# Kernel optimization log

Measured on AMD Instinct MI355X. Metric: run time of the kernel, lower is better.

## Reference

```python
import jax, jax.numpy as jnp
import numpy as np
from functools import partial

NUM_HEADS = 12
RATIO_ACT = 0.5   # prune_ratio_act_store
RATIO_ATTN = 0.5  # prune_ratio_attn_mat_store


def kth_mask(x, ratio):
    # torch.kthvalue semantics: threshold = k-th SMALLEST of |x| over the flat tensor
    n = x.size
    k = int(np.clip(n * ratio, 1, n))
    mag = jnp.abs(x)
    thr = jnp.sort(mag.reshape(-1))[k - 1]
    return (mag >= thr).astype(x.dtype)


def st(dense, prune):
    # straight-through: value = dense, gradient flows through `prune` path
    return jax.lax.stop_gradient(dense) + prune - jax.lax.stop_gradient(prune)


def _softmax_prune_impl(x, ratio):
    dense = jax.nn.softmax(x, axis=-1)
    mask = kth_mask(dense, ratio)
    return dense, mask * dense


@partial(jax.custom_vjp, nondiff_argnums=(1,))
def softmax_prune(x, ratio):
    return _softmax_prune_impl(x, ratio)


def _sp_fwd(x, ratio):
    dense, sparse = _softmax_prune_impl(x, ratio)
    return (dense, sparse), sparse


def _sp_bwd(ratio, A, cots):
    # custom backward uses the SPARSE probs in the softmax Jacobian; the
    # cotangent of the sparse output is ignored (matches the torch Function)
    g_dense, _ = cots
    g = A * (g_dense - jnp.sum(g_dense * A, axis=-1, keepdims=True))
    return (g,)


softmax_prune.defvjp(_sp_fwd, _sp_bwd)


def setup_inputs() -> dict:
    key = jax.random.key(0)
    ks = jax.random.split(key, 5)
    B, S, H = 8, 577, 768
    hs = jax.random.normal(ks[0], (B, S, H), dtype=jnp.float32)
    w = lambda k: jax.random.normal(k, (H, H), dtype=jnp.float32) * 0.02
    z = jnp.zeros((H,), dtype=jnp.float32)
    return {
        "hidden_states": hs,
        "Wq": w(ks[1]), "bq": z,
        "Wk": w(ks[2]), "bk": z,
        "Wv": w(ks[3]), "bv": z,
        "Wo": w(ks[4]), "bo": z,
    }


def attention_forward(hidden_states, Wq, bq, Wk, bk, Wv, bv, Wo, bo):
    B, S, H = hidden_states.shape
    nh, hd = NUM_HEADS, H // NUM_HEADS
    sg = jax.lax.stop_gradient
    lin = lambda x, W, b: x @ W + b

    # prune hidden states by global magnitude threshold
    hs_p = sg(kth_mask(hidden_states, RATIO_ACT)) * hidden_states

    q = st(lin(hidden_states, Wq, bq), lin(hs_p, Wq, bq))
    k = st(lin(hidden_states, Wk, bk), lin(hs_p, Wk, bk))
    v = st(lin(hidden_states, Wv, bv), lin(hs_p, Wv, bv))

    heads = lambda x: x.reshape(B, S, nh, hd).transpose(0, 2, 1, 3)  # [B,h,S,d]
    q, k, v = heads(q), heads(k), heads(v)

    qp = sg(kth_mask(q, RATIO_ACT)) * q
    kp = sg(kth_mask(k, RATIO_ACT)) * k

    scores = st(jnp.einsum('bhqd,bhkd->bhqk', q, k),
                jnp.einsum('bhqd,bhkd->bhqk', qp, kp))
    scores = scores / float(np.sqrt(hd))

    probs, probs_p = softmax_prune(scores, RATIO_ATTN)  # dropout rate = 0 -> identity

    vp = sg(kth_mask(v, RATIO_ACT)) * v
    ctx = st(jnp.einsum('bhqk,bhkd->bhqd', probs, v),
             jnp.einsum('bhqk,bhkd->bhqd', probs_p, vp))

    ctx = ctx.transpose(0, 2, 1, 3).reshape(B, S, H)
    ctx_p = sg(kth_mask(ctx, RATIO_ACT)) * ctx

    out = st(lin(ctx, Wo, bo), lin(ctx_p, Wo, bo))
    return out  # vis=False -> weights is None


def reference(hidden_states, Wq, bq, Wk, bk, Wv, bv, Wo, bo):
    return attention_forward(hidden_states, Wq, bq, Wk, bk, Wv, bv, Wo, bo)
```

## Files before the change

kernel.cpp:

```cpp
#include <hip/hip_runtime.h>
#include <hip/hip_bf16.h>


#define B_ 8
#define S_ 577
#define H_ 768
#define NH_ 12
#define HD_ 64
#define M_ (B_*S_)
#define MPAD 4736
#define BH_ (B_*NH_)
#define SKPAD 640
#define LTS 136
#define LTS2 264

typedef __attribute__((ext_vector_type(8))) short short8;
typedef __attribute__((ext_vector_type(4))) short s16x4;
typedef __attribute__((ext_vector_type(4))) float f32x4;

__device__ inline unsigned short f2bf(float f){
    unsigned int u = __float_as_uint(f);
    u = u + 0x7fffu + ((u>>16)&1u);
    return (unsigned short)(u>>16);
}

__device__ inline void gload_lds16(const short* g, short* l){
    __builtin_amdgcn_global_load_lds((const __attribute__((address_space(1))) void*)g,
                                     (__attribute__((address_space(3))) void*)l, 16, 0, 0);
}

__global__ __launch_bounds__(256) void k_prep(
    const float* __restrict__ hs, short* __restrict__ abf,
    const float* __restrict__ Wq, const float* __restrict__ Wk,
    const float* __restrict__ Wv, const float* __restrict__ Wo,
    short* __restrict__ Tq, short* __restrict__ Tk,
    short* __restrict__ Tv, short* __restrict__ To,
    short* __restrict__ kh, short* __restrict__ vt)
{
    const int bid = blockIdx.x, t = threadIdx.x;
    if(bid < 1776){
        int i = bid*256 + t;
        if(bid >= 1731){ *(short8*)(abf + (size_t)i*8) = (short8){}; return; }
        const float4* p = (const float4*)(hs + (size_t)i*8);
        float4 a = p[0], b = p[1];
        short8 v;
        v[0]=(short)f2bf(a.x); v[1]=(short)f2bf(a.y); v[2]=(short)f2bf(a.z); v[3]=(short)f2bf(a.w);
        v[4]=(short)f2bf(b.x); v[5]=(short)f2bf(b.y); v[6]=(short)f2bf(b.z); v[7]=(short)f2bf(b.w);
        *(short8*)(abf + (size_t)i*8) = v;
    } else if(bid < 2352){
        int zidx = bid - 1776;
        int z = zidx & 3, rem = zidx >> 2;
        int kx = rem % 12, ny = rem / 12;
        const float* W = z==0?Wq: z==1?Wk: z==2?Wv:Wo;
        short*       T = z==0?Tq: z==1?Tk: z==2?Tv:To;
        __shared__ float lds[64][65];
        int k0 = kx*64, n0 = ny*64;
        for(int i=0;i<4;i++){
            int row = i*16 + (t>>4);
            int col = (t&15)*4;
            float4 v = *(const float4*)&W[(k0+row)*768 + n0 + col];
            lds[row][col]=v.x; lds[row][col+1]=v.y; lds[row][col+2]=v.z; lds[row][col+3]=v.w;
        }
        __syncthreads();
        for(int i=0;i<4;i++){
            int n = i*16 + (t>>4);
            int k4 = (t&15)*4;
            for(int j=0;j<4;j++)
                T[(n0+n)*768 + k0 + k4 + j] = (short)f2bf(lds[k4+j][n]);
        }
    } else {
        int tid = (bid-2352)*256 + t;
        short8 z = {};
        if(tid < 48384){
            int row_id = tid>>3, ch = tid&7;
            int bh = row_id/63, r = row_id - bh*63;
            *(short8*)&kh[((size_t)bh*SKPAD + 577 + r)*64 + ch*8] = z;
        } else if(tid < 97536){
            int j = tid - 48384;
            int row_id = j>>3, ch = j&7;
            int bh = row_id>>6, d = row_id&63;
            *(short8*)&vt[((size_t)bh*64 + d)*SKPAD + 576 + ch*8] = z;
        }
    }
}

__global__ __launch_bounds__(512) void k_qkv(
    const short* __restrict__ A, const short* __restrict__ T,
    const float* __restrict__ b0, const float* __restrict__ b1, const float* __restrict__ b2,
    short* __restrict__ oq, short* __restrict__ ok, short* __restrict__ ovt)
{
    __shared__ short sh[65536];
    const int t = threadIdx.x;

    const int nwg = gridDim.x;
    const int q8 = nwg>>3, r8 = nwg&7;
    const int xcd = blockIdx.x&7, cidx = blockIdx.x>>3;
    const int wg = (xcd<r8 ? xcd*(q8+1) : r8*(q8+1) + (xcd-r8)*q8) + cidx;
    const int mt = wg/9, nt9 = wg - mt*9;
    const int m0 = mt*256, n0 = nt9*256;
    const int seg = n0/768;
    const float* bias = (seg==0?b0: seg==1?b1:b2);
    const int nlb = n0 - seg*768;

    const int w = t>>6, lane = t&63, g = lane>>4, c = lane&15;
    const int wm = w>>2, wn = w&3;

    const int srow = t>>3, sch = t&7;
    const int sx = (sch ^ (srow&7))*8;
    const short* pa[2][2]; const short* pb[2][2];
    #pragma unroll
    for(int hf=0; hf<2; hf++)
        #pragma unroll
        for(int i=0;i<2;i++){
            int rga = m0 + hf*128 + i*64 + srow;
            if(rga > 4735) rga = 4735;
            pa[hf][i] = A + (size_t)rga*768 + sx;
            pb[hf][i] = T + (size_t)(n0 + hf*128 + i*64 + srow)*768 + sx;
        }
    const int dof = srow*64 + sch*8;

    f32x4 acc[8][4] = {};

    #define STAGE(tt) { int pS = ((tt)&1)*16384; int kof = (tt)*64;              \
        _Pragma("unroll") for(int hf=0; hf<2; hf++){                             \
            _Pragma("unroll") for(int i=0;i<2;i++){                              \
                gload_lds16(pa[hf][i] + kof, &sh[pS + hf*8192 + i*4096 + dof]);  \
                gload_lds16(pb[hf][i] + kof, &sh[32768 + pS + hf*8192 + i*4096 + dof]); } } }

    STAGE(0);
    asm volatile("s_waitcnt vmcnt(0)" ::: "memory");
    __builtin_amdgcn_s_barrier();
    asm volatile("" ::: "memory");

    for(int kt=0; kt<12; kt++){
        const int p = (kt&1)*16384;
        const short* LA = &sh[p + wm*8192];
        const short* LB = &sh[32768 + p + (wn>>1)*8192];
        const int brow0 = (wn&1)*64;

        short8 af[4][2], af2[4][2], bfv[4][2];
        #pragma unroll
        for(int mi=0; mi<4; mi++){
            int rih = mi*16 + c, rx = (rih&7)<<3;
            af[mi][0] = *(const short8*)&LA[rih*64 + ((g*8) ^ rx)];
            af[mi][1] = *(const short8*)&LA[rih*64 + ((32+g*8) ^ rx)];
        }
        #pragma unroll
        for(int ni=0; ni<2; ni++){
            int rih = brow0 + ni*16 + c, rx = (rih&7)<<3;
            bfv[ni][0] = *(const short8*)&LB[rih*64 + ((g*8) ^ rx)];
            bfv[ni][1] = *(const short8*)&LB[rih*64 + ((32+g*8) ^ rx)];
        }
        if(kt < 11) STAGE(kt+1);
        __builtin_amdgcn_s_barrier();
        asm volatile("s_waitcnt lgkmcnt(0)" ::: "memory");
        __builtin_amdgcn_s_setprio(1);
        #pragma unroll
        for(int mi=0; mi<4; mi++)
            #pragma unroll
            for(int ni=0; ni<2; ni++){
                acc[mi][ni] = __builtin_amdgcn_mfma_f32_16x16x32_bf16(af[mi][0], bfv[ni][0], acc[mi][ni], 0,0,0);
                acc[mi][ni] = __builtin_amdgcn_mfma_f32_16x16x32_bf16(af[mi][1], bfv[ni][1], acc[mi][ni], 0,0,0);
            }
        __builtin_amdgcn_s_setprio(0);
        __builtin_amdgcn_s_barrier();
        asm volatile("" ::: "memory");

        #pragma unroll
        for(int ni=2; ni<4; ni++){
            int rih = brow0 + ni*16 + c, rx = (rih&7)<<3;
            bfv[ni][0] = *(const short8*)&LB[rih*64 + ((g*8) ^ rx)];
            bfv[ni][1] = *(const short8*)&LB[rih*64 + ((32+g*8) ^ rx)];
        }
        __builtin_amdgcn_s_barrier();
        asm volatile("s_waitcnt lgkmcnt(0)" ::: "memory");
        __builtin_amdgcn_s_setprio(1);
        #pragma unroll
        for(int mi=0; mi<4; mi++)
            #pragma unroll
            for(int ni=2; ni<4; ni++){
                acc[mi][ni] = __builtin_amdgcn_mfma_f32_16x16x32_bf16(af[mi][0], bfv[ni][0], acc[mi][ni], 0,0,0);
                acc[mi][ni] = __builtin_amdgcn_mfma_f32_16x16x32_bf16(af[mi][1], bfv[ni][1], acc[mi][ni], 0,0,0);
            }
        __builtin_amdgcn_s_setprio(0);
        __builtin_amdgcn_s_barrier();
        asm volatile("" ::: "memory");

        #pragma unroll
        for(int mi=0; mi<4; mi++){
            int rih = 64 + mi*16 + c, rx = (rih&7)<<3;
            af2[mi][0] = *(const short8*)&LA[rih*64 + ((g*8) ^ rx)];
            af2[mi][1] = *(const short8*)&LA[rih*64 + ((32+g*8) ^ rx)];
        }
        __builtin_amdgcn_s_barrier();
        asm volatile("s_waitcnt lgkmcnt(0)" ::: "memory");
        __builtin_amdgcn_s_setprio(1);
        #pragma unroll
        for(int mi=0; mi<4; mi++)
            #pragma unroll
            for(int ni=0; ni<2; ni++){
                acc[4+mi][ni] = __builtin_amdgcn_mfma_f32_16x16x32_bf16(af2[mi][0], bfv[ni][0], acc[4+mi][ni], 0,0,0);
                acc[4+mi][ni] = __builtin_amdgcn_mfma_f32_16x16x32_bf16(af2[mi][1], bfv[ni][1], acc[4+mi][ni], 0,0,0);
            }
        __builtin_amdgcn_s_setprio(0);
        __builtin_amdgcn_s_barrier();
        asm volatile("" ::: "memory");

        __builtin_amdgcn_s_setprio(1);
        #pragma unroll
        for(int mi=0; mi<4; mi++)
            #pragma unroll
            for(int ni=2; ni<4; ni++){
                acc[4+mi][ni] = __builtin_amdgcn_mfma_f32_16x16x32_bf16(af2[mi][0], bfv[ni][0], acc[4+mi][ni], 0,0,0);
                acc[4+mi][ni] = __builtin_amdgcn_mfma_f32_16x16x32_bf16(af2[mi][1], bfv[ni][1], acc[4+mi][ni], 0,0,0);
            }
        __builtin_amdgcn_s_setprio(0);
        asm volatile("s_waitcnt vmcnt(0)" ::: "memory");
        __builtin_amdgcn_s_barrier();
        asm volatile("" ::: "memory");
    }
    #undef STAGE

    if(seg==2){
        #pragma unroll
        for(int cch=0; cch<2; cch++){
            if((wn>>1) == cch){
                #pragma unroll
                for(int mi=0; mi<8; mi++)
                    #pragma unroll
                    for(int ni=0; ni<4; ni++){
                        int nc = (wn&1)*64 + ni*16 + c;
                        float bv = bias[nlb + cch*128 + nc];
                        s16x4 pk;
                        #pragma unroll
                        for(int r=0;r<4;r++) pk[r] = (short)f2bf(acc[mi][ni][r] + bv);
                        int ml0 = wm*128 + mi*16 + g*4;
                        *(s16x4*)&sh[nc*LTS2 + ml0] = pk;
                    }
            }
            __syncthreads();
            #pragma unroll
            for(int i=0;i<8;i++){
                int idx = i*512 + t;
                int rp = idx>>5, ch = idx&31;
                short8 v8 = *(const short8*)&sh[rp*LTS2 + ch*8];
                int nl = nlb + cch*128 + rp, hh = nl>>6, dd = nl&63;
                int mg = m0 + ch*8;
                if(mg < M_){
                    int bb = mg/S_, s0 = mg - bb*S_;
                    if(s0+7 < S_ && mg+7 < M_){
                        *(short8*)&ovt[(((size_t)bb*NH_+hh)*HD_+dd)*SKPAD + s0] = v8;
                    } else {
                        for(int j=0;j<8;j++){
                            int m=mg+j;
                            if(m<M_){ int bj=m/S_, sj=m-bj*S_;
                                ovt[(((size_t)bj*NH_+hh)*HD_+dd)*SKPAD+sj]=v8[j]; }
                        }
                    }
                }
            }
            __syncthreads();
        }
    } else {
        #pragma unroll
        for(int cch=0; cch<2; cch++){
            if(wm == cch){
                #pragma unroll
                for(int mi=0; mi<8; mi++)
                    #pragma unroll
                    for(int ni=0; ni<4; ni++){
                        int nl_ = wn*64 + ni*16 + c;
                        float bv = bias[nlb + nl_];
                        #pragma unroll
                        for(int r=0;r<4;r++){
                            int ml = mi*16 + g*4 + r;
                            sh[ml*LTS2 + nl_] = (short)f2bf(acc[mi][ni][r] + bv);
                        }
                    }
            }
            __syncthreads();
            #pragma unroll
            for(int i=0;i<8;i++){
                int idx = i*512 + t;
                int rp = idx>>5, ch = idx&31;
                short8 v8 = *(const short8*)&sh[rp*LTS2 + ch*8];
                int m = m0 + cch*128 + rp;
                if(m < M_){
                    int bb = m/S_, ss = m - bb*S_;
                    int nl = nlb + ch*8, hh = nl>>6, dd = nl&63;
                    if(seg==1) *(short8*)&ok[(((size_t)bb*NH_+hh)*SKPAD + ss)*HD_ + dd] = v8;
                    else       *(short8*)&oq[(((size_t)bb*NH_+hh)*S_   + ss)*HD_ + dd] = v8;
                }
            }
            __syncthreads();
        }
    }
}

__global__ __launch_bounds__(512) void k_gemm(
    const short* __restrict__ A, const short* __restrict__ T,
    const float* __restrict__ b0,
    float* __restrict__ of, int NT)
{
    __shared__ short sh[32768];
    const int t = threadIdx.x;

    const int nwg = gridDim.x;
    const int q8 = nwg>>3, r8 = nwg&7;
    const int xcd = blockIdx.x&7, cidx = blockIdx.x>>3;
    const int wg = (xcd<r8 ? xcd*(q8+1) : r8*(q8+1) + (xcd-r8)*q8) + cidx;
    const int mt = wg/NT, ntile = wg - mt*NT;
    const int m0 = mt*128, n0 = ntile*128;
    const float* bias = b0;

    const int w = t>>6, lane = t&63, g = lane>>4, c = lane&15;
    const int wm = w>>1, wn = w&1;

    const int lrow = lane>>3;
    const int lcol = ((lane&7) ^ lrow) * 8;
    const short* pa = A + (size_t)(m0 + w*8 + lrow)*768 + lcol;
    const short* pb = T + (size_t)(n0 + w*8 + lrow)*768 + lcol;

    f32x4 acc[2][4] = {};

    #pragma unroll
    for(int i=0;i<2;i++){
        gload_lds16(pa + (size_t)(i*64)*768, &sh[(i*64 + w*8)*64]);
        gload_lds16(pb + (size_t)(i*64)*768, &sh[8192 + (i*64 + w*8)*64]);
    }
    int bb = 0;
    for(int kk=0; kk<12; kk++){
        if(kk<11){
            short* dstA = &sh[(bb^1)*16384];
            short* dstB = dstA + 8192;
            #pragma unroll
            for(int i=0;i<2;i++){
                gload_lds16(pa + (size_t)(i*64)*768 + (kk+1)*64, &dstA[(i*64 + w*8)*64]);
                gload_lds16(pb + (size_t)(i*64)*768 + (kk+1)*64, &dstB[(i*64 + w*8)*64]);
            }
            asm volatile("s_waitcnt vmcnt(4)" ::: "memory");
        } else {
            asm volatile("s_waitcnt vmcnt(0)" ::: "memory");
        }
        __builtin_amdgcn_s_barrier();
        asm volatile("" ::: "memory");

        const short* LA = &sh[bb*16384];
        const short* LB = LA + 8192;
        short8 af[2][2], bfv[4][2];
        #pragma unroll
        for(int mi=0; mi<2; mi++){
            int row = wm*32 + mi*16 + c;
            int rx = (row&7)<<3;
            af[mi][0] = *(const short8*)&LA[row*64 + ((g*8) ^ rx)];
            af[mi][1] = *(const short8*)&LA[row*64 + ((32 + g*8) ^ rx)];
        }
        #pragma unroll
        for(int ni=0; ni<4; ni++){
            int row = wn*64 + ni*16 + c;
            int rx = (row&7)<<3;
            bfv[ni][0] = *(const short8*)&LB[row*64 + ((g*8) ^ rx)];
            bfv[ni][1] = *(const short8*)&LB[row*64 + ((32 + g*8) ^ rx)];
        }
        __builtin_amdgcn_s_setprio(1);
        #pragma unroll
        for(int mi=0; mi<2; mi++)
            #pragma unroll
            for(int ni=0; ni<4; ni++){
                acc[mi][ni] = __builtin_amdgcn_mfma_f32_16x16x32_bf16(af[mi][0], bfv[ni][0], acc[mi][ni], 0,0,0);
                acc[mi][ni] = __builtin_amdgcn_mfma_f32_16x16x32_bf16(af[mi][1], bfv[ni][1], acc[mi][ni], 0,0,0);
            }
        __builtin_amdgcn_s_setprio(0);
        asm volatile("s_waitcnt lgkmcnt(0)" ::: "memory");
        __builtin_amdgcn_s_barrier();
        asm volatile("" ::: "memory");
        bb ^= 1;
    }

    #pragma unroll
    for(int mi=0; mi<2; mi++) for(int ni=0; ni<4; ni++){
        #pragma unroll
        for(int r=0; r<4; r++){
            int m = m0 + wm*32 + mi*16 + g*4 + r;
            int n = n0 + wn*64 + ni*16 + c;
            if(m >= M_) continue;
            of[(size_t)m*768 + n] = acc[mi][ni][r] + bias[n];
        }
    }
}

__global__ __launch_bounds__(256) void k_attn(
    const short* __restrict__ qh, const short* __restrict__ kh, const short* __restrict__ vt,
    short* __restrict__ ctx)
{
    __shared__ short lK[2][64*64], lV[2][64*64], lP[4*2048];
    const int t = threadIdx.x;
    const int w = t>>6, lane = t&63, g = lane>>4, c = lane&15;
    const int bh = blockIdx.x, b = bh/NH_, h = bh%NH_;
    const int q0 = blockIdx.y*128;

    #pragma unroll
    for(int i=0;i<4;i++){
        int row = i*8 + (lane>>3);
        int e8 = (lane&7)*8;
        int s = q0 + w*32 + row;
        short8 v = {};
        if(s < S_) v = *(const short8*)&qh[((size_t)bh*S_ + s)*HD_ + e8];
        *(short8*)&lP[w*2048 + row*64 + (e8 ^ ((row&7)<<3))] = v;
    }
    short8 qf[2][2];
    #pragma unroll
    for(int qi=0; qi<2; qi++)
        #pragma unroll
        for(int ks=0; ks<2; ks++)
            qf[qi][ks] = *(const short8*)&lP[w*2048 + (qi*16+c)*64 + ((ks*32+g*8) ^ ((c&7)<<3))];

    short8 ones;
    #pragma unroll
    for(int j=0;j<8;j++) ones[j] = (short)0x3F80;

    const int srow = lane>>3;
    const int sw8 = ((lane&7) ^ srow)*8;
    const short* pk0 = kh + ((size_t)bh*SKPAD + w*16 + srow)*64 + sw8;
    const short* pv0 = vt + ((size_t)bh*64 + w*16 + srow)*SKPAD + sw8;

    #pragma unroll
    for(int i=0;i<2;i++){
        gload_lds16(pk0 + i*8*64,    &lK[0][(w*16+i*8)*64]);
        gload_lds16(pv0 + i*8*SKPAD, &lV[0][(w*16+i*8)*64]);
    }

    float m_run[2][4], l_run[2][4];
    f32x4 O[2][4] = {};
    #pragma unroll
    for(int qi=0;qi<2;qi++)
        #pragma unroll
        for(int r=0;r<4;r++){ m_run[qi][r] = -3e38f; l_run[qi][r] = 0.f; }

    int bb = 0;
    for(int kt=0; kt<10; kt++){
        if(kt<9){
            const short* pk = pk0 + (kt+1)*4096;
            const short* pv = pv0 + (kt+1)*64;
            #pragma unroll
            for(int i=0;i<2;i++){
                gload_lds16(pk + i*8*64,    &lK[bb^1][(w*16+i*8)*64]);
                gload_lds16(pv + i*8*SKPAD, &lV[bb^1][(w*16+i*8)*64]);
            }
            asm volatile("s_waitcnt vmcnt(4)" ::: "memory");
        } else {
            asm volatile("s_waitcnt vmcnt(0)" ::: "memory");
        }
        __builtin_amdgcn_s_barrier();
        asm volatile("" ::: "memory");

        const short* LK = lK[bb]; const short* LV = lV[bb];

        float sv[2][4][4];
        #pragma unroll
        for(int nt=0; nt<4; nt++){
            int row = nt*16 + c;
            int rx = (row&7)<<3;
            short8 kf[2];
            kf[0] = *(const short8*)&LK[row*64 + ((g*8) ^ rx)];
            kf[1] = *(const short8*)&LK[row*64 + ((32+g*8) ^ rx)];
            __builtin_amdgcn_s_setprio(1);
            #pragma unroll
            for(int qi=0; qi<2; qi++){
                f32x4 sa = {};
                sa = __builtin_amdgcn_mfma_f32_16x16x32_bf16(qf[qi][0], kf[0], sa, 0,0,0);
                sa = __builtin_amdgcn_mfma_f32_16x16x32_bf16(qf[qi][1], kf[1], sa, 0,0,0);
                #pragma unroll
                for(int r=0;r<4;r++) sv[qi][nt][r] = sa[r]*0.18033688011f;
            }
            __builtin_amdgcn_s_setprio(0);
        }
        if(kt==9){
            #pragma unroll
            for(int nt=0; nt<4; nt++){
                int key = 576 + nt*16 + c;
                if(key >= S_){
                    #pragma unroll
                    for(int qi=0;qi<2;qi++)
                        #pragma unroll
                        for(int r=0;r<4;r++) sv[qi][nt][r] = -3e38f;
                }
            }
        }
        float fac[2][4];
        #pragma unroll
        for(int qi=0; qi<2; qi++)
            #pragma unroll
            for(int r=0;r<4;r++){
                float mx = fmaxf(fmaxf(sv[qi][0][r],sv[qi][1][r]),fmaxf(sv[qi][2][r],sv[qi][3][r]));
                for(int off=1; off<16; off<<=1) mx = fmaxf(mx, __shfl_xor(mx, off));
                float nm = fmaxf(m_run[qi][r], mx);
                fac[qi][r] = __builtin_amdgcn_exp2f(m_run[qi][r] - nm);
                m_run[qi][r] = nm;
            }
        #pragma unroll
        for(int qi=0; qi<2; qi++)
            #pragma unroll
            for(int nt=0; nt<4; nt++)
                #pragma unroll
                for(int r=0;r<4;r++){
                    float p = __builtin_amdgcn_exp2f(sv[qi][nt][r] - m_run[qi][r]);
                    int prow = g*4 + r;
                    lP[w*2048 + qi*1024 + prow*64 + ((nt*16 + c) ^ ((prow&7)<<3))] = (short)f2bf(p);
                }
        short8 pf[2][2];
        #pragma unroll
        for(int qi=0; qi<2; qi++)
            #pragma unroll
            for(int ks=0; ks<2; ks++)
                pf[qi][ks] = *(const short8*)&lP[w*2048 + qi*1024 + c*64 + ((ks*32+g*8) ^ ((c&7)<<3))];
        __builtin_amdgcn_s_setprio(1);
        #pragma unroll
        for(int qi=0; qi<2; qi++){
            f32x4 rs = {};
            rs = __builtin_amdgcn_mfma_f32_16x16x32_bf16(pf[qi][0], ones, rs, 0,0,0);
            rs = __builtin_amdgcn_mfma_f32_16x16x32_bf16(pf[qi][1], ones, rs, 0,0,0);
            #pragma unroll
            for(int r=0;r<4;r++) l_run[qi][r] = l_run[qi][r]*fac[qi][r] + rs[r];
        }
        __builtin_amdgcn_s_setprio(0);
        #pragma unroll
        for(int qi=0; qi<2; qi++)
            #pragma unroll
            for(int nt=0;nt<4;nt++)
                #pragma unroll
                for(int r=0;r<4;r++) O[qi][nt][r] *= fac[qi][r];

        __builtin_amdgcn_s_setprio(1);
        #pragma unroll
        for(int nt=0; nt<4; nt++){
            int vrow = nt*16 + c;
            int rx = (vrow&7)<<3;
            short8 vf[2];
            vf[0] = *(const short8*)&LV[vrow*64 + ((g*8) ^ rx)];
            vf[1] = *(const short8*)&LV[vrow*64 + ((32+g*8) ^ rx)];
            #pragma unroll
            for(int qi=0; qi<2; qi++){
                O[qi][nt] = __builtin_amdgcn_mfma_f32_16x16x32_bf16(pf[qi][0], vf[0], O[qi][nt], 0,0,0);
                O[qi][nt] = __builtin_amdgcn_mfma_f32_16x16x32_bf16(pf[qi][1], vf[1], O[qi][nt], 0,0,0);
            }
        }
        __builtin_amdgcn_s_setprio(0);
        asm volatile("s_waitcnt lgkmcnt(0)" ::: "memory");
        __builtin_amdgcn_s_barrier();
        asm volatile("" ::: "memory");
        bb ^= 1;
    }

    #pragma unroll
    for(int qi=0; qi<2; qi++)
        #pragma unroll
        for(int nt=0; nt<4; nt++)
            #pragma unroll
            for(int r=0;r<4;r++){
                int s = q0 + w*32 + qi*16 + g*4 + r;
                if(s < S_){
                    float val = O[qi][nt][r] / l_run[qi][r];
                    ctx[((size_t)b*S_ + s)*H_ + h*HD_ + nt*16 + c] = (short)f2bf(val);
                }
            }
}

extern "C" void kernel_launch(void* const* d_in, const int* in_sizes, int n_in,
                              void* d_out, int out_size, void* d_ws, size_t ws_size,
                              hipStream_t stream)
{
    const float* hs = (const float*)d_in[0];
    const float* Wq = (const float*)d_in[1];
    const float* bq = (const float*)d_in[2];
    const float* Wk = (const float*)d_in[3];
    const float* bk = (const float*)d_in[4];
    const float* Wv = (const float*)d_in[5];
    const float* bv = (const float*)d_in[6];
    const float* Wo = (const float*)d_in[7];
    const float* bo = (const float*)d_in[8];
    float* out = (float*)d_out;

    char* ws = (char*)d_ws;
    short* abf = (short*)(ws);
    short* ctx = abf;
    short* wqt = (short*)(ws + 7274496);
    short* wkt = (short*)(ws + 7274496 + 1179648);
    short* wvt = (short*)(ws + 7274496 + 2*1179648);
    short* wot = (short*)(ws + 7274496 + 3*1179648);
    short* qh  = (short*)(ws + 11993088);
    short* kh  = (short*)(ws + 19083264);
    short* vt  = (short*)(ws + 26947584);

    k_prep<<<2733, 256, 0, stream>>>(hs, abf, Wq,Wk,Wv,Wo, wqt,wkt,wvt,wot, kh, vt);
    k_qkv<<<171, 512, 0, stream>>>(abf, wqt, bq,bk,bv, qh,kh,vt);
    k_attn<<<dim3(96,5), 256, 0, stream>>>(qh, kh, vt, ctx);
    k_gemm<<<222, 512, 0, stream>>>(ctx, wot, bo, out, 6);
}
```

Measured before the change: 97.67 us.

## Switch QKV GEMM to triple-buffered K=32 stages with interleaved async loads

```diff
diff --git a/kernel.cpp b/kernel.cpp
--- a/kernel.cpp
+++ b/kernel.cpp
@@ -89,7 +89,7 @@
     const float* __restrict__ b0, const float* __restrict__ b1, const float* __restrict__ b2,
     short* __restrict__ oq, short* __restrict__ ok, short* __restrict__ ovt)
 {
-    __shared__ short sh[65536];
+    __shared__ short sh[49152];
     const int t = threadIdx.x;
 
     const int nwg = gridDim.x;
@@ -105,121 +105,115 @@
     const int w = t>>6, lane = t&63, g = lane>>4, c = lane&15;
     const int wm = w>>2, wn = w&3;
 
-    const int srow = t>>3, sch = t&7;
-    const int sx = (sch ^ (srow&7))*8;
-    const short* pa[2][2]; const short* pb[2][2];
-    #pragma unroll
-    for(int hf=0; hf<2; hf++)
-        #pragma unroll
-        for(int i=0;i<2;i++){
-            int rga = m0 + hf*128 + i*64 + srow;
-            if(rga > 4735) rga = 4735;
-            pa[hf][i] = A + (size_t)rga*768 + sx;
-            pb[hf][i] = T + (size_t)(n0 + hf*128 + i*64 + srow)*768 + sx;
-        }
-    const int dof = srow*64 + sch*8;
+    const short *gA0,*gA1,*gB0,*gB1; int dA0,dA1,dB0,dB1;
+    {
+        int cid0 = t,      r0 = cid0>>2, c0 = cid0&3;
+        int cid1 = 512+t,  r1 = cid1>>2, c1 = cid1&3;
+        int rga0 = m0+r0; if(rga0>4735) rga0 = 4735;
+        int rga1 = m0+r1; if(rga1>4735) rga1 = 4735;
+        gA0 = A + (size_t)rga0*768 + (c0 ^ ((r0>>1)&3))*8;
+        gA1 = A + (size_t)rga1*768 + (c1 ^ ((r1>>1)&3))*8;
+        gB0 = T + (size_t)(n0+r0)*768 + (c0 ^ ((r0>>1)&3))*8;
+        gB1 = T + (size_t)(n0+r1)*768 + (c1 ^ ((r1>>1)&3))*8;
+        dA0 = r0*32 + c0*8; dA1 = r1*32 + c1*8;
+        dB0 = 8192 + dA0;   dB1 = 8192 + dA1;
+    }
+    #define SLOT(tt) (((tt)%3)*16384)
+    #define ISSA0(tt) gload_lds16(gA0 + (tt)*32, &sh[SLOT(tt) + dA0])
+    #define ISSA1(tt) gload_lds16(gA1 + (tt)*32, &sh[SLOT(tt) + dA1])
+    #define ISSB0(tt) gload_lds16(gB0 + (tt)*32, &sh[SLOT(tt) + dB0])
+    #define ISSB1(tt) gload_lds16(gB1 + (tt)*32, &sh[SLOT(tt) + dB1])
 
     f32x4 acc[8][4] = {};
 
-    #define STAGE(tt) { int pS = ((tt)&1)*16384; int kof = (tt)*64;              \
-        _Pragma("unroll") for(int hf=0; hf<2; hf++){                             \
-            _Pragma("unroll") for(int i=0;i<2;i++){                              \
-                gload_lds16(pa[hf][i] + kof, &sh[pS + hf*8192 + i*4096 + dof]);  \
-                gload_lds16(pb[hf][i] + kof, &sh[32768 + pS + hf*8192 + i*4096 + dof]); } } }
-
-    STAGE(0);
-    asm volatile("s_waitcnt vmcnt(0)" ::: "memory");
+    ISSA0(0); ISSA1(0); ISSB0(0); ISSB1(0);
+    ISSA0(1); ISSA1(1); ISSB0(1); ISSB1(1);
+    asm volatile("s_waitcnt vmcnt(4)" ::: "memory");
     __builtin_amdgcn_s_barrier();
     asm volatile("" ::: "memory");
 
-    for(int kt=0; kt<12; kt++){
-        const int p = (kt&1)*16384;
-        const short* LA = &sh[p + wm*8192];
-        const short* LB = &sh[32768 + p + (wn>>1)*8192];
-        const int brow0 = (wn&1)*64;
-
-        short8 af[4][2], af2[4][2], bfv[4][2];
+    for(int kt=0; kt<24; kt++){
+        const short* LA = &sh[SLOT(kt)];
+        const short* LB = LA + 8192;
+        short8 a[4], a2[4], b[4];
+
         #pragma unroll
         for(int mi=0; mi<4; mi++){
-            int rih = mi*16 + c, rx = (rih&7)<<3;
-            af[mi][0] = *(const short8*)&LA[rih*64 + ((g*8) ^ rx)];
-            af[mi][1] = *(const short8*)&LA[rih*64 + ((32+g*8) ^ rx)];
+            int row = wm*128 + mi*16 + c;
+            a[mi] = *(const short8*)&LA[row*32 + ((g ^ ((row>>1)&3))<<3)];
         }
         #pragma unroll
         for(int ni=0; ni<2; ni++){
-            int rih = brow0 + ni*16 + c, rx = (rih&7)<<3;
-            bfv[ni][0] = *(const short8*)&LB[rih*64 + ((g*8) ^ rx)];
-            bfv[ni][1] = *(const short8*)&LB[rih*64 + ((32+g*8) ^ rx)];
-        }
-        if(kt < 11) STAGE(kt+1);
+            int row = wn*64 + ni*16 + c;
+            b[ni] = *(const short8*)&LB[row*32 + ((g ^ ((row>>1)&3))<<3)];
+        }
+        if(kt<22) ISSA0(kt+2);
         __builtin_amdgcn_s_barrier();
         asm volatile("s_waitcnt lgkmcnt(0)" ::: "memory");
         __builtin_amdgcn_s_setprio(1);
         #pragma unroll
         for(int mi=0; mi<4; mi++)
             #pragma unroll
-            for(int ni=0; ni<2; ni++){
-                acc[mi][ni] = __builtin_amdgcn_mfma_f32_16x16x32_bf16(af[mi][0], bfv[ni][0], acc[mi][ni], 0,0,0);
-                acc[mi][ni] = __builtin_amdgcn_mfma_f32_16x16x32_bf16(af[mi][1], bfv[ni][1], acc[mi][ni], 0,0,0);
-            }
+            for(int ni=0; ni<2; ni++)
+                acc[mi][ni] = __builtin_amdgcn_mfma_f32_16x16x32_bf16(a[mi], b[ni], acc[mi][ni],0,0,0);
         __builtin_amdgcn_s_setprio(0);
         __builtin_amdgcn_s_barrier();
         asm volatile("" ::: "memory");
 
         #pragma unroll
         for(int ni=2; ni<4; ni++){
-            int rih = brow0 + ni*16 + c, rx = (rih&7)<<3;
-            bfv[ni][0] = *(const short8*)&LB[rih*64 + ((g*8) ^ rx)];
-            bfv[ni][1] = *(const short8*)&LB[rih*64 + ((32+g*8) ^ rx)];
-        }
+            int row = wn*64 + ni*16 + c;
+            b[ni] = *(const short8*)&LB[row*32 + ((g ^ ((row>>1)&3))<<3)];
+        }
+        if(kt<22) ISSA1(kt+2);
         __builtin_amdgcn_s_barrier();
         asm volatile("s_waitcnt lgkmcnt(0)" ::: "memory");
         __builtin_amdgcn_s_setprio(1);
         #pragma unroll
         for(int mi=0; mi<4; mi++)
             #pragma unroll
-            for(int ni=2; ni<4; ni++){
-                acc[mi][ni] = __builtin_amdgcn_mfma_f32_16x16x32_bf16(af[mi][0], bfv[ni][0], acc[mi][ni], 0,0,0);
-                acc[mi][ni] = __builtin_amdgcn_mfma_f32_16x16x32_bf16(af[mi][1], bfv[ni][1], acc[mi][ni], 0,0,0);
-            }
+            for(int ni=2; ni<4; ni++)
+                acc[mi][ni] = __builtin_amdgcn_mfma_f32_16x16x32_bf16(a[mi], b[ni], acc[mi][ni],0,0,0);
         __builtin_amdgcn_s_setprio(0);
         __builtin_amdgcn_s_barrier();
         asm volatile("" ::: "memory");
 
         #pragma unroll
         for(int mi=0; mi<4; mi++){
-            int rih = 64 + mi*16 + c, rx = (rih&7)<<3;
-            af2[mi][0] = *(const short8*)&LA[rih*64 + ((g*8) ^ rx)];
-            af2[mi][1] = *(const short8*)&LA[rih*64 + ((32+g*8) ^ rx)];
-        }
+            int row = wm*128 + 64 + mi*16 + c;
+            a2[mi] = *(const short8*)&LA[row*32 + ((g ^ ((row>>1)&3))<<3)];
+        }
+        if(kt<22) ISSB0(kt+2);
         __builtin_amdgcn_s_barrier();
         asm volatile("s_waitcnt lgkmcnt(0)" ::: "memory");
         __builtin_amdgcn_s_setprio(1);
         #pragma unroll
         for(int mi=0; mi<4; mi++)
             #pragma unroll
-            for(int ni=0; ni<2; ni++){
-                acc[4+mi][ni] = __builtin_amdgcn_mfma_f32_16x16x32_bf16(af2[mi][0], bfv[ni][0], acc[4+mi][ni], 0,0,0);
-                acc[4+mi][ni] = __builtin_amdgcn_mfma_f32_16x16x32_bf16(af2[mi][1], bfv[ni][1], acc[4+mi][ni], 0,0,0);
-            }
-        __builtin_amdgcn_s_setprio(0);
-        __builtin_amdgcn_s_barrier();
-        asm volatile("" ::: "memory");
-
+            for(int ni=0; ni<2; ni++)
+                acc[4+mi][ni] = __builtin_amdgcn_mfma_f32_16x16x32_bf16(a2[mi], b[ni], acc[4+mi][ni],0,0,0);
+        __builtin_amdgcn_s_setprio(0);
+        __builtin_amdgcn_s_barrier();
+        asm volatile("" ::: "memory");
+
+        if(kt<22) ISSB1(kt+2);
         __builtin_amdgcn_s_setprio(1);
         #pragma unroll
         for(int mi=0; mi<4; mi++)
             #pragma unroll
-            for(int ni=2; ni<4; ni++){
-                acc[4+mi][ni] = __builtin_amdgcn_mfma_f32_16x16x32_bf16(af2[mi][0], bfv[ni][0], acc[4+mi][ni], 0,0,0);
-                acc[4+mi][ni] = __builtin_amdgcn_mfma_f32_16x16x32_bf16(af2[mi][1], bfv[ni][1], acc[4+mi][ni], 0,0,0);
-            }
-        __builtin_amdgcn_s_setprio(0);
-        asm volatile("s_waitcnt vmcnt(0)" ::: "memory");
-        __builtin_amdgcn_s_barrier();
-        asm volatile("" ::: "memory");
-    }
-    #undef STAGE
+            for(int ni=2; ni<4; ni++)
+                acc[4+mi][ni] = __builtin_amdgcn_mfma_f32_16x16x32_bf16(a2[mi], b[ni], acc[4+mi][ni],0,0,0);
+        __builtin_amdgcn_s_setprio(0);
+        if(kt<22){ asm volatile("s_waitcnt vmcnt(4)" ::: "memory"); }
+        else     { asm volatile("s_waitcnt vmcnt(0)" ::: "memory"); }
+        __builtin_amdgcn_s_barrier();
+        asm volatile("" ::: "memory");
+    }
+    #undef SLOT
+    #undef ISSA0
+    #undef ISSA1
+    #undef ISSB0
+    #undef ISSB1
 
     if(seg==2){
         #pragma unroll
```

Result: slower. 100.2 us (+2.5%).
